# Performance work log

Hardware: AMD Instinct MI355X
Metric: run time of the kernel (lower is better)

## Reference

```python
import jax, jax.numpy as jnp
import numpy as np

N_NODES = 50000
N_EDGES = 800000
IN_DIM = 128
HID_DIM = 128
N_CLASSES = 64


def gcn_conv(x, edge_index, W, b):
    """PyG GCNConv: add self-loops, sym deg^-1/2 norm, xW, scatter-add, +bias."""
    n = x.shape[0]
    loop = jnp.arange(n, dtype=edge_index.dtype)
    src = jnp.concatenate([edge_index[0], loop])  # [E+N]
    dst = jnp.concatenate([edge_index[1], loop])  # [E+N]
    ones = jnp.ones(src.shape[0], dtype=x.dtype)
    deg = jax.ops.segment_sum(ones, dst, num_segments=n)  # in-degree incl self-loop
    dinv = jnp.where(deg > 0, jax.lax.rsqrt(deg), jnp.zeros_like(deg))
    norm = dinv[src] * dinv[dst]  # [E+N]
    h = x @ W  # [N, out]
    msg = h[src] * norm[:, None]  # [E+N, out] gather + scale
    out = jax.ops.segment_sum(msg, dst, num_segments=n)  # scatter-add
    return out + b


def setup_inputs() -> dict:
    key = jax.random.key(0)
    k1, k2, k3, k4, k5 = jax.random.split(key, 5)
    x = jax.random.normal(k1, (N_NODES, IN_DIM), dtype=jnp.float32)
    edge_index = jax.random.randint(k2, (2, N_EDGES), 0, N_NODES, dtype=jnp.int64)
    # Glorot-style init for the two GCNConv linear weights; zero biases (PyG default)
    s1 = 1.0 / np.sqrt(IN_DIM)
    s2 = 1.0 / np.sqrt(HID_DIM)
    W1 = jax.random.uniform(k3, (IN_DIM, HID_DIM), jnp.float32, -s1, s1)
    b1 = jnp.zeros((HID_DIM,), jnp.float32)
    W2 = jax.random.uniform(k4, (HID_DIM, N_CLASSES), jnp.float32, -s2, s2)
    b2 = jnp.zeros((N_CLASSES,), jnp.float32)
    return {"x": x, "edge_index": edge_index, "W1": W1, "b1": b1, "W2": W2, "b2": b2}


def reference(x, edge_index, W1, b1, W2, b2):
    h = gcn_conv(x, edge_index, W1, b1)
    h = jax.nn.relu(h)
    out = gcn_conv(h, edge_index, W2, b2)
    return out
```

## Files before the change

### kernel.cpp

```cpp
#include <hip/hip_runtime.h>
#include <hip/hip_bf16.h>
#include <hip/hip_fp16.h>


#define NODES_PER_BLOCK 4
#define CHUNK 4096
#define BCAP 8192

typedef unsigned int uint;
typedef _Float16 f16x8 __attribute__((ext_vector_type(8)));
typedef float f32x4 __attribute__((ext_vector_type(4)));

__device__ __forceinline__ float2 h2f(uint v) {
  __half2 h;
  __builtin_memcpy(&h, &v, 4);
  return __half22float2(h);
}

__device__ __forceinline__ uint f2h(float a, float b) {
  __half2 h = __halves2half2(__float2half_rn(a), __float2half_rn(b));
  uint r;
  __builtin_memcpy(&r, &h, 4);
  return r;
}

__global__ void detect64_k(const int* ei, int* flag) {
  int lane = threadIdx.x & 63;
  unsigned long long m = __ballot(ei[2 * lane + 1] != 0);
  if (threadIdx.x == 0) *flag = (m == 0ULL) ? 1 : 0;
}

__global__ __launch_bounds__(256) void hist_k(const int* __restrict__ ei,
                                              const int* __restrict__ flag,
                                              int* __restrict__ gh,
                                              int E, int nchunk, int nbuck) {
  __shared__ int h[256];
  int c = blockIdx.x;
  for (int i = threadIdx.x; i < 256; i += 256) h[i] = 0;
  __syncthreads();
  int is64 = *flag;
  int base = c * CHUNK;
  int lim = min(CHUNK, E - base);
  for (int i = threadIdx.x; i < lim; i += 256) {
    int e = base + i;
    int d = is64 ? ei[2 * ((size_t)E + e)] : ei[(size_t)E + e];
    atomicAdd(&h[d >> 8], 1);
  }
  __syncthreads();
  for (int k = threadIdx.x; k < nbuck; k += 256) gh[k * nchunk + c] = h[k];
}

__global__ __launch_bounds__(256) void tot_k(const int* __restrict__ gh,
                                             int* __restrict__ totals, int nchunk) {
  __shared__ int sd[256];
  int k = blockIdx.x;
  int s = 0;
  for (int i = threadIdx.x; i < nchunk; i += 256) s += gh[k * nchunk + i];
  sd[threadIdx.x] = s;
  __syncthreads();
  for (int o = 128; o > 0; o >>= 1) {
    if (threadIdx.x < o) sd[threadIdx.x] += sd[threadIdx.x + o];
    __syncthreads();
  }
  if (threadIdx.x == 0) totals[k] = sd[0];
}

__global__ __launch_bounds__(256) void scanrow_k(int* __restrict__ gh,
                                                 const int* __restrict__ totals,
                                                 int* __restrict__ bucketStart,
                                                 int* __restrict__ offsets,
                                                 int nchunk, int nbuck, int N, int E) {
  __shared__ int st[256];
  int k = blockIdx.x;
  int t = threadIdx.x;
  int v = (t < nbuck && t < k) ? totals[t] : 0;
  st[t] = v;
  __syncthreads();
  for (int o = 128; o > 0; o >>= 1) {
    if (t < o) st[t] += st[t + o];
    __syncthreads();
  }
  int bs = st[0];
  if (t == 0) {
    bucketStart[k] = bs;
    if (k == nbuck - 1) { bucketStart[nbuck] = E; offsets[N] = E; }
  }
  __syncthreads();
  int x = (t < nchunk) ? gh[k * nchunk + t] : 0;
  st[t] = x;
  __syncthreads();
  int incl = x;
  for (int o = 1; o < 256; o <<= 1) {
    int add = (t >= o) ? st[t - o] : 0;
    __syncthreads();
    incl += add;
    st[t] = incl;
    __syncthreads();
  }
  if (t < nchunk) gh[k * nchunk + t] = bs + (incl - x);
}

__global__ __launch_bounds__(256) void part_k(const int* __restrict__ ei,
                                              const int* __restrict__ flag,
                                              const int* __restrict__ gh,
                                              int* __restrict__ tmp,
                                              int E, int nchunk, int nbuck) {
  __shared__ int cur[256];
  int c = blockIdx.x;
  for (int i = threadIdx.x; i < nbuck; i += 256) cur[i] = gh[i * nchunk + c];
  __syncthreads();
  int is64 = *flag;
  int base = c * CHUNK;
  int lim = min(CHUNK, E - base);
  for (int i = threadIdx.x; i < lim; i += 256) {
    int e = base + i;
    int s, d;
    if (is64) {
      s = ei[2 * (size_t)e];
      d = ei[2 * ((size_t)E + e)];
    } else {
      s = ei[e];
      d = ei[(size_t)E + e];
    }
    int p = atomicAdd(&cur[d >> 8], 1);
    tmp[p] = s | ((d & 255) << 16);
  }
}

__global__ __launch_bounds__(256) void bucket_k(const int* __restrict__ tmp,
                                                const int* __restrict__ bucketStart,
                                                int* __restrict__ csr_src,
                                                int* __restrict__ offsets,
                                                float* __restrict__ dinv,
                                                int N) {
  __shared__ int ebuf[BCAP];
  __shared__ int cnt[256];
  __shared__ int st[256];
  __shared__ int lofs[256];
  int k = blockIdx.x;
  int b0 = bucketStart[k], b1 = bucketStart[k + 1];
  int sz = b1 - b0;
  int t = threadIdx.x;
  cnt[t] = 0;
  __syncthreads();
  bool inlds = (sz <= BCAP);
  if (inlds) {
    for (int i = t; i < sz; i += 256) {
      int v = tmp[b0 + i];
      ebuf[i] = v;
      atomicAdd(&cnt[v >> 16], 1);
    }
  } else {
    for (int i = t; i < sz; i += 256) atomicAdd(&cnt[tmp[b0 + i] >> 16], 1);
  }
  __syncthreads();
  int x = cnt[t];
  st[t] = x;
  __syncthreads();
  int incl = x;
  for (int o = 1; o < 256; o <<= 1) {
    int add = (t >= o) ? st[t - o] : 0;
    __syncthreads();
    incl += add;
    st[t] = incl;
    __syncthreads();
  }
  lofs[t] = incl - x;
  int node = k * 256 + t;
  if (node < N) {
    offsets[node] = b0 + lofs[t];
    dinv[node] = rsqrtf((float)(x + 1));
  }
  __syncthreads();
  cnt[t] = lofs[t];
  __syncthreads();
  if (inlds) {
    for (int i = t; i < sz; i += 256) {
      int v = ebuf[i];
      int p = atomicAdd(&cnt[v >> 16], 1);
      csr_src[b0 + p] = v & 0xFFFF;
    }
  } else {
    for (int i = t; i < sz; i += 256) {
      int v = tmp[b0 + i];
      int p = atomicAdd(&cnt[v >> 16], 1);
      csr_src[b0 + p] = v & 0xFFFF;
    }
  }
}

__global__ void prep_k(const float* __restrict__ W, _Float16* __restrict__ P,
                       int NC, int total) {
  int idx = blockIdx.x * blockDim.x + threadIdx.x;
  if (idx >= total) return;
  int NF = NC >> 4;
  int j = idx & 7;
  int l = (idx >> 3) & 63;
  int rest = idx >> 9;
  int c = rest % NF;
  int t = rest / NF;
  int k = t * 32 + ((l >> 4) << 3) + j;
  int col = c * 16 + (l & 15);
  P[idx] = (_Float16)W[(size_t)k * NC + col];
}

template <int NC, bool A16>
__global__ __launch_bounds__(256) void mfma_gemm_k(const void* __restrict__ Xv,
                                                   const _Float16* __restrict__ Wp,
                                                   const float* __restrict__ dinv,
                                                   _Float16* __restrict__ H, int M) {
  constexpr int NF = NC / 16;
  int lane = threadIdx.x & 63;
  int w = threadIdx.x >> 6;
  int row0 = blockIdx.x * 64 + w * 16;
  int arow = row0 + (lane & 15);
  bool av = arow < M;
  const uint4* wp = (const uint4*)Wp;

  f32x4 acc[NF];
#pragma unroll
  for (int c = 0; c < NF; ++c) acc[c] = (f32x4){0.f, 0.f, 0.f, 0.f};

#pragma unroll
  for (int t = 0; t < 4; ++t) {
    f16x8 a;
    if constexpr (A16) {
      const _Float16* xr = (const _Float16*)Xv + (size_t)arow * 128 + ((lane >> 4) << 3);
      uint4 araw = av ? *(const uint4*)(xr + t * 32)
                      : make_uint4(0u, 0u, 0u, 0u);
      __builtin_memcpy(&a, &araw, 16);
    } else {
      const float* xr = (const float*)Xv + (size_t)arow * 128 + ((lane >> 4) << 3);
      float4 lo = av ? *(const float4*)(xr + t * 32)
                     : make_float4(0.f, 0.f, 0.f, 0.f);
      float4 hi = av ? *(const float4*)(xr + t * 32 + 4)
                     : make_float4(0.f, 0.f, 0.f, 0.f);
      a[0] = (_Float16)lo.x; a[1] = (_Float16)lo.y;
      a[2] = (_Float16)lo.z; a[3] = (_Float16)lo.w;
      a[4] = (_Float16)hi.x; a[5] = (_Float16)hi.y;
      a[6] = (_Float16)hi.z; a[7] = (_Float16)hi.w;
    }
#pragma unroll
    for (int c = 0; c < NF; ++c) {
      uint4 braw = wp[(t * NF + c) * 64 + lane];
      f16x8 b;
      __builtin_memcpy(&b, &braw, 16);
      acc[c] = __builtin_amdgcn_mfma_f32_16x16x32_f16(a, b, acc[c], 0, 0, 0);
    }
  }

  int rbase = row0 + ((lane >> 4) << 2);
#pragma unroll
  for (int r = 0; r < 4; ++r) {
    int row = rbase + r;
    if (row < M) {
      float di = dinv[row];
#pragma unroll
      for (int c = 0; c < NF; ++c)
        H[(size_t)row * NC + c * 16 + (lane & 15)] = (_Float16)(di * acc[c][r]);
    }
  }
}

__global__ __launch_bounds__(256) void agg1_k(const uint* __restrict__ hp,
                                              const float* __restrict__ dinv,
                                              const int* __restrict__ offsets,
                                              const int* __restrict__ csr_src,
                                              const float* __restrict__ b,
                                              uint* __restrict__ y, int n) {
  int wave = threadIdx.x >> 6;
  int lane = threadIdx.x & 63;
  int node = blockIdx.x * NODES_PER_BLOCK + wave;
  if (node >= n) return;
  int beg = offsets[node], end = offsets[node + 1];
  int deg = end - beg;
  float2 self = h2f(hp[(size_t)node * 64 + lane]);
  float ax = self.x, ay = self.y;
  int sv = 0;
  if (lane < deg) sv = csr_src[beg + lane];
  int lim = deg < 64 ? deg : 64;
  int e = 0;
  for (; e + 8 <= lim; e += 8) {
    int s0 = __shfl(sv, e + 0), s1 = __shfl(sv, e + 1);
    int s2 = __shfl(sv, e + 2), s3 = __shfl(sv, e + 3);
    int s4 = __shfl(sv, e + 4), s5 = __shfl(sv, e + 5);
    int s6 = __shfl(sv, e + 6), s7 = __shfl(sv, e + 7);
    uint u0 = hp[(size_t)s0 * 64 + lane];
    uint u1 = hp[(size_t)s1 * 64 + lane];
    uint u2 = hp[(size_t)s2 * 64 + lane];
    uint u3 = hp[(size_t)s3 * 64 + lane];
    uint u4 = hp[(size_t)s4 * 64 + lane];
    uint u5 = hp[(size_t)s5 * 64 + lane];
    uint u6 = hp[(size_t)s6 * 64 + lane];
    uint u7 = hp[(size_t)s7 * 64 + lane];
    float2 v0 = h2f(u0), v1 = h2f(u1), v2 = h2f(u2), v3 = h2f(u3);
    float2 v4 = h2f(u4), v5 = h2f(u5), v6 = h2f(u6), v7 = h2f(u7);
    ax += ((v0.x + v1.x) + (v2.x + v3.x)) + ((v4.x + v5.x) + (v6.x + v7.x));
    ay += ((v0.y + v1.y) + (v2.y + v3.y)) + ((v4.y + v5.y) + (v6.y + v7.y));
  }
  for (; e < lim; ++e) {
    int s = __shfl(sv, e);
    float2 v = h2f(hp[(size_t)s * 64 + lane]);
    ax += v.x;
    ay += v.y;
  }
  for (int ee = beg + 64; ee < end; ++ee) {
    float2 v = h2f(hp[(size_t)csr_src[ee] * 64 + lane]);
    ax += v.x;
    ay += v.y;
  }
  float di = dinv[node];
  float2 bb = ((const float2*)b)[lane];
  float ox = fmaxf(fmaf(di, ax, bb.x), 0.0f);
  float oy = fmaxf(fmaf(di, ay, bb.y), 0.0f);
  y[(size_t)node * 64 + lane] = f2h(ox, oy);
}

__global__ __launch_bounds__(256) void agg2_k(const uint* __restrict__ hp,
                                              const float* __restrict__ dinv,
                                              const int* __restrict__ offsets,
                                              const int* __restrict__ csr_src,
                                              const float* __restrict__ b,
                                              float* __restrict__ out, int n) {
  int wv = threadIdx.x >> 6;
  int lane = threadIdx.x & 63;
  int half = lane >> 5;
  int fl = lane & 31;
  int node = blockIdx.x * 8 + wv * 2 + half;
  if (node >= n) return;
  int beg = offsets[node], end = offsets[node + 1];
  int deg = end - beg;
  float2 self = h2f(hp[(size_t)node * 32 + fl]);
  float ax = self.x, ay = self.y;
  int sv = 0;
  if (fl < deg) sv = csr_src[beg + fl];
  int lim = deg < 32 ? deg : 32;
  int e = 0;
  for (; e + 8 <= lim; e += 8) {
    int s0 = __shfl(sv, e + 0, 32), s1 = __shfl(sv, e + 1, 32);
    int s2 = __shfl(sv, e + 2, 32), s3 = __shfl(sv, e + 3, 32);
    int s4 = __shfl(sv, e + 4, 32), s5 = __shfl(sv, e + 5, 32);
    int s6 = __shfl(sv, e + 6, 32), s7 = __shfl(sv, e + 7, 32);
    uint u0 = hp[(size_t)s0 * 32 + fl];
    uint u1 = hp[(size_t)s1 * 32 + fl];
    uint u2 = hp[(size_t)s2 * 32 + fl];
    uint u3 = hp[(size_t)s3 * 32 + fl];
    uint u4 = hp[(size_t)s4 * 32 + fl];
    uint u5 = hp[(size_t)s5 * 32 + fl];
    uint u6 = hp[(size_t)s6 * 32 + fl];
    uint u7 = hp[(size_t)s7 * 32 + fl];
    float2 v0 = h2f(u0), v1 = h2f(u1), v2 = h2f(u2), v3 = h2f(u3);
    float2 v4 = h2f(u4), v5 = h2f(u5), v6 = h2f(u6), v7 = h2f(u7);
    ax += ((v0.x + v1.x) + (v2.x + v3.x)) + ((v4.x + v5.x) + (v6.x + v7.x));
    ay += ((v0.y + v1.y) + (v2.y + v3.y)) + ((v4.y + v5.y) + (v6.y + v7.y));
  }
  for (; e < lim; ++e) {
    int s = __shfl(sv, e, 32);
    float2 v = h2f(hp[(size_t)s * 32 + fl]);
    ax += v.x;
    ay += v.y;
  }
  for (int ee = beg + 32; ee < end; ++ee) {
    float2 v = h2f(hp[(size_t)csr_src[ee] * 32 + fl]);
    ax += v.x;
    ay += v.y;
  }
  float di = dinv[node];
  float2 bb = ((const float2*)b)[fl];
  float2 o;
  o.x = fmaf(di, ax, bb.x);
  o.y = fmaf(di, ay, bb.y);
  ((float2*)out)[(size_t)node * 32 + fl] = o;
}

extern "C" void kernel_launch(void* const* d_in, const int* in_sizes, int n_in,
                              void* d_out, int out_size, void* d_ws, size_t ws_size,
                              hipStream_t stream) {
  const float* x  = (const float*)d_in[0];
  const int*   ei = (const int*)d_in[1];
  const float* W1 = (const float*)d_in[2];
  const float* b1 = (const float*)d_in[3];
  const float* W2 = (const float*)d_in[4];
  const float* b2 = (const float*)d_in[5];
  float* out = (float*)d_out;

  const int N = in_sizes[0] / 128;
  const int E = in_sizes[1] / 2;
  const int NBUCK = (N + 255) >> 8;
  const int NCHUNK = (E + CHUNK - 1) / CHUNK;

  char* w = (char*)d_ws;
  size_t off = 0;
  auto alloc = [&](size_t bytes) -> void* {
    void* p = w + off;
    off = (off + bytes + 511) & ~(size_t)511;
    return p;
  };
  int*       gh      = (int*)alloc((size_t)NBUCK * NCHUNK * 4);
  int*       totals  = (int*)alloc((size_t)NBUCK * 4);
  int*       bstart  = (int*)alloc((size_t)(NBUCK + 1) * 4);
  int*       flag    = (int*)alloc(64);
  int*       tmp     = (int*)alloc((size_t)E * 4);
  int*       offsets = (int*)alloc((size_t)(N + 1) * 4);
  float*     dinv    = (float*)alloc((size_t)N * 4);
  int*       csr_src = (int*)alloc((size_t)E * 4);
  _Float16*  pW1     = (_Float16*)alloc(16384 * 2);
  _Float16*  pW2     = (_Float16*)alloc(8192 * 2);
  _Float16*  h1      = (_Float16*)alloc((size_t)N * 128 * 2);
  _Float16*  y       = (_Float16*)alloc((size_t)N * 128 * 2);
  _Float16*  h2      = (_Float16*)alloc((size_t)N * 64 * 2);

  const int GB  = (N + 63) / 64;
  const int AB  = (N + NODES_PER_BLOCK - 1) / NODES_PER_BLOCK;
  const int AB2 = (N + 7) / 8;

  detect64_k<<<1, 64, 0, stream>>>(ei, flag);
  hist_k<<<NCHUNK, 256, 0, stream>>>(ei, flag, gh, E, NCHUNK, NBUCK);
  tot_k<<<NBUCK, 256, 0, stream>>>(gh, totals, NCHUNK);
  scanrow_k<<<NBUCK, 256, 0, stream>>>(gh, totals, bstart, offsets, NCHUNK, NBUCK, N, E);
  part_k<<<NCHUNK, 256, 0, stream>>>(ei, flag, gh, tmp, E, NCHUNK, NBUCK);
  bucket_k<<<NBUCK, 256, 0, stream>>>(tmp, bstart, csr_src, offsets, dinv, N);

  prep_k<<<64, 256, 0, stream>>>(W1, pW1, 128, 16384);
  prep_k<<<32, 256, 0, stream>>>(W2, pW2, 64, 8192);

  mfma_gemm_k<128, false><<<GB, 256, 0, stream>>>(x, pW1, dinv, h1, N);
  agg1_k<<<AB, 256, 0, stream>>>((const uint*)h1, dinv, offsets, csr_src, b1,
                                 (uint*)y, N);
  mfma_gemm_k<64, true><<<GB, 256, 0, stream>>>(y, pW2, dinv, h2, N);
  agg2_k<<<AB2, 256, 0, stream>>>((const uint*)h2, dinv, offsets, csr_src, b2, out, N);
}
```

Measured before the change: 118.0 us.

## Column-chunk feature layout for aggregation, smaller buckets, fuse detect and prep kernels

Stores the GEMM outputs in 32-column chunks (chunk-major), so each gather row is 64 bytes and the chunks can be aggregated by separate blocks. A single templated aggregation kernel replaces the two old ones: four lane groups each handle a different edge and are combined with shuffles. CSR bucket size drops from 256 to 128 nodes, the int64 detection is folded into hist and part, and the two weight-prep kernels are merged. This cuts launch count and spreads the gather over more blocks, at the cost of more grid blocks and extra shuffle reductions.

```diff
diff --git a/kernel.cpp b/kernel.cpp
--- a/kernel.cpp
+++ b/kernel.cpp
@@ -3,9 +3,10 @@
 #include <hip/hip_fp16.h>
 
 
-#define NODES_PER_BLOCK 4
 #define CHUNK 4096
-#define BCAP 8192
+#define BSHIFT 7
+#define BSIZE 128
+#define BCAP 4096
 
 typedef unsigned int uint;
 typedef _Float16 f16x8 __attribute__((ext_vector_type(8)));
@@ -24,27 +25,29 @@
   return r;
 }
 
-__global__ void detect64_k(const int* ei, int* flag) {
-  int lane = threadIdx.x & 63;
-  unsigned long long m = __ballot(ei[2 * lane + 1] != 0);
-  if (threadIdx.x == 0) *flag = (m == 0ULL) ? 1 : 0;
+__device__ __forceinline__ int block_is64(const int* ei, int* s_is64) {
+  if (threadIdx.x < 64) {
+    unsigned long long m = __ballot(ei[2 * threadIdx.x + 1] != 0);
+    if (threadIdx.x == 0) *s_is64 = (m == 0ULL) ? 1 : 0;
+  }
+  __syncthreads();
+  return *s_is64;
 }
 
 __global__ __launch_bounds__(256) void hist_k(const int* __restrict__ ei,
-                                              const int* __restrict__ flag,
                                               int* __restrict__ gh,
                                               int E, int nchunk, int nbuck) {
-  __shared__ int h[256];
+  __shared__ int h[512];
+  __shared__ int s_is64;
   int c = blockIdx.x;
-  for (int i = threadIdx.x; i < 256; i += 256) h[i] = 0;
-  __syncthreads();
-  int is64 = *flag;
+  for (int i = threadIdx.x; i < 512; i += 256) h[i] = 0;
+  int is64 = block_is64(ei, &s_is64);
   int base = c * CHUNK;
   int lim = min(CHUNK, E - base);
   for (int i = threadIdx.x; i < lim; i += 256) {
     int e = base + i;
     int d = is64 ? ei[2 * ((size_t)E + e)] : ei[(size_t)E + e];
-    atomicAdd(&h[d >> 8], 1);
+    atomicAdd(&h[d >> BSHIFT], 1);
   }
   __syncthreads();
   for (int k = threadIdx.x; k < nbuck; k += 256) gh[k * nchunk + c] = h[k];
@@ -73,8 +76,9 @@
   __shared__ int st[256];
   int k = blockIdx.x;
   int t = threadIdx.x;
-  int v = (t < nbuck && t < k) ? totals[t] : 0;
-  st[t] = v;
+  int partial = 0;
+  for (int i = t; i < k; i += 256) partial += totals[i];
+  st[t] = partial;
   __syncthreads();
   for (int o = 128; o > 0; o >>= 1) {
     if (t < o) st[t] += st[t + o];
@@ -101,15 +105,14 @@
 }
 
 __global__ __launch_bounds__(256) void part_k(const int* __restrict__ ei,
-                                              const int* __restrict__ flag,
                                               const int* __restrict__ gh,
                                               int* __restrict__ tmp,
                                               int E, int nchunk, int nbuck) {
-  __shared__ int cur[256];
+  __shared__ int cur[512];
+  __shared__ int s_is64;
   int c = blockIdx.x;
   for (int i = threadIdx.x; i < nbuck; i += 256) cur[i] = gh[i * nchunk + c];
-  __syncthreads();
-  int is64 = *flag;
+  int is64 = block_is64(ei, &s_is64);
   int base = c * CHUNK;
   int lim = min(CHUNK, E - base);
   for (int i = threadIdx.x; i < lim; i += 256) {
@@ -122,8 +125,8 @@
       s = ei[e];
       d = ei[(size_t)E + e];
     }
-    int p = atomicAdd(&cur[d >> 8], 1);
-    tmp[p] = s | ((d & 255) << 16);
+    int p = atomicAdd(&cur[d >> BSHIFT], 1);
+    tmp[p] = s | ((d & (BSIZE - 1)) << 16);
   }
 }
 
@@ -134,14 +137,14 @@
                                                 float* __restrict__ dinv,
                                                 int N) {
   __shared__ int ebuf[BCAP];
-  __shared__ int cnt[256];
+  __shared__ int cnt[BSIZE];
   __shared__ int st[256];
-  __shared__ int lofs[256];
+  __shared__ int lofs[BSIZE];
   int k = blockIdx.x;
   int b0 = bucketStart[k], b1 = bucketStart[k + 1];
   int sz = b1 - b0;
   int t = threadIdx.x;
-  cnt[t] = 0;
+  if (t < BSIZE) cnt[t] = 0;
   __syncthreads();
   bool inlds = (sz <= BCAP);
   if (inlds) {
@@ -154,7 +157,7 @@
     for (int i = t; i < sz; i += 256) atomicAdd(&cnt[tmp[b0 + i] >> 16], 1);
   }
   __syncthreads();
-  int x = cnt[t];
+  int x = (t < BSIZE) ? cnt[t] : 0;
   st[t] = x;
   __syncthreads();
   int incl = x;
@@ -165,14 +168,16 @@
     st[t] = incl;
     __syncthreads();
   }
-  lofs[t] = incl - x;
-  int node = k * 256 + t;
-  if (node < N) {
-    offsets[node] = b0 + lofs[t];
-    dinv[node] = rsqrtf((float)(x + 1));
-  }
-  __syncthreads();
-  cnt[t] = lofs[t];
+  int node = (k << BSHIFT) + t;
+  if (t < BSIZE) {
+    lofs[t] = incl - x;
+    if (node < N) {
+      offsets[node] = b0 + lofs[t];
+      dinv[node] = rsqrtf((float)(x + 1));
+    }
+  }
+  __syncthreads();
+  if (t < BSIZE) cnt[t] = lofs[t];
   __syncthreads();
   if (inlds) {
     for (int i = t; i < sz; i += 256) {
@@ -189,19 +194,25 @@
   }
 }
 
-__global__ void prep_k(const float* __restrict__ W, _Float16* __restrict__ P,
-                       int NC, int total) {
+__global__ void prep2_k(const float* __restrict__ W1,
+                        const float* __restrict__ W2,
+                        _Float16* __restrict__ P) {
   int idx = blockIdx.x * blockDim.x + threadIdx.x;
-  if (idx >= total) return;
+  if (idx >= 24576) return;
+  const float* W;
+  _Float16* dst;
+  int NC, li;
+  if (idx < 16384) { W = W1; dst = P;        NC = 128; li = idx; }
+  else             { W = W2; dst = P + 16384; NC = 64;  li = idx - 16384; }
   int NF = NC >> 4;
-  int j = idx & 7;
-  int l = (idx >> 3) & 63;
-  int rest = idx >> 9;
+  int j = li & 7;
+  int l = (li >> 3) & 63;
+  int rest = li >> 9;
   int c = rest % NF;
   int t = rest / NF;
   int k = t * 32 + ((l >> 4) << 3) + j;
   int col = c * 16 + (l & 15);
-  P[idx] = (_Float16)W[(size_t)k * NC + col];
+  dst[li] = (_Float16)W[(size_t)k * NC + col];
 }
 
 template <int NC, bool A16>
@@ -225,16 +236,15 @@
   for (int t = 0; t < 4; ++t) {
     f16x8 a;
     if constexpr (A16) {
-      const _Float16* xr = (const _Float16*)Xv + (size_t)arow * 128 + ((lane >> 4) << 3);
-      uint4 araw = av ? *(const uint4*)(xr + t * 32)
-                      : make_uint4(0u, 0u, 0u, 0u);
+      const _Float16* yr =
+          (const _Float16*)Xv + ((size_t)t * M + arow) * 32 + ((lane >> 4) << 3);
+      uint4 araw = av ? *(const uint4*)yr : make_uint4(0u, 0u, 0u, 0u);
       __builtin_memcpy(&a, &araw, 16);
     } else {
-      const float* xr = (const float*)Xv + (size_t)arow * 128 + ((lane >> 4) << 3);
-      float4 lo = av ? *(const float4*)(xr + t * 32)
-                     : make_float4(0.f, 0.f, 0.f, 0.f);
-      float4 hi = av ? *(const float4*)(xr + t * 32 + 4)
-                     : make_float4(0.f, 0.f, 0.f, 0.f);
+      const float* xr =
+          (const float*)Xv + (size_t)arow * 128 + ((lane >> 4) << 3) + t * 32;
+      float4 lo = av ? *(const float4*)xr : make_float4(0.f, 0.f, 0.f, 0.f);
+      float4 hi = av ? *(const float4*)(xr + 4) : make_float4(0.f, 0.f, 0.f, 0.f);
       a[0] = (_Float16)lo.x; a[1] = (_Float16)lo.y;
       a[2] = (_Float16)lo.z; a[3] = (_Float16)lo.w;
       a[4] = (_Float16)hi.x; a[5] = (_Float16)hi.y;
@@ -256,121 +266,82 @@
     if (row < M) {
       float di = dinv[row];
 #pragma unroll
-      for (int c = 0; c < NF; ++c)
-        H[(size_t)row * NC + c * 16 + (lane & 15)] = (_Float16)(di * acc[c][r]);
-    }
-  }
-}
-
-__global__ __launch_bounds__(256) void agg1_k(const uint* __restrict__ hp,
-                                              const float* __restrict__ dinv,
-                                              const int* __restrict__ offsets,
-                                              const int* __restrict__ csr_src,
-                                              const float* __restrict__ b,
-                                              uint* __restrict__ y, int n) {
+      for (int c = 0; c < NF; ++c) {
+        size_t off = ((size_t)(c >> 1) * M + row) * 32 + (c & 1) * 16 + (lane & 15);
+        H[off] = (_Float16)(di * acc[c][r]);
+      }
+    }
+  }
+}
+
+template <bool RELU, bool OUT16>
+__global__ __launch_bounds__(256) void agg_k(const uint* __restrict__ hp,
+                                             const float* __restrict__ dinv,
+                                             const int* __restrict__ offsets,
+                                             const int* __restrict__ csr_src,
+                                             const float* __restrict__ b,
+                                             void* __restrict__ outv,
+                                             int n, int nblk, int ncfull) {
   int wave = threadIdx.x >> 6;
   int lane = threadIdx.x & 63;
-  int node = blockIdx.x * NODES_PER_BLOCK + wave;
+  int c = blockIdx.x / nblk;
+  int nb = blockIdx.x % nblk;
+  int node = nb * 4 + wave;
   if (node >= n) return;
+  int g = lane >> 4;
+  int j = lane & 15;
   int beg = offsets[node], end = offsets[node + 1];
   int deg = end - beg;
-  float2 self = h2f(hp[(size_t)node * 64 + lane]);
-  float ax = self.x, ay = self.y;
+  const uint* hc = hp + (size_t)c * n * 16;
+  float ax = 0.f, ay = 0.f;
+  if (g == 0) {
+    float2 s = h2f(hc[(size_t)node * 16 + j]);
+    ax = s.x; ay = s.y;
+  }
   int sv = 0;
   if (lane < deg) sv = csr_src[beg + lane];
   int lim = deg < 64 ? deg : 64;
-  int e = 0;
-  for (; e + 8 <= lim; e += 8) {
-    int s0 = __shfl(sv, e + 0), s1 = __shfl(sv, e + 1);
-    int s2 = __shfl(sv, e + 2), s3 = __shfl(sv, e + 3);
-    int s4 = __shfl(sv, e + 4), s5 = __shfl(sv, e + 5);
-    int s6 = __shfl(sv, e + 6), s7 = __shfl(sv, e + 7);
-    uint u0 = hp[(size_t)s0 * 64 + lane];
-    uint u1 = hp[(size_t)s1 * 64 + lane];
-    uint u2 = hp[(size_t)s2 * 64 + lane];
-    uint u3 = hp[(size_t)s3 * 64 + lane];
-    uint u4 = hp[(size_t)s4 * 64 + lane];
-    uint u5 = hp[(size_t)s5 * 64 + lane];
-    uint u6 = hp[(size_t)s6 * 64 + lane];
-    uint u7 = hp[(size_t)s7 * 64 + lane];
-    float2 v0 = h2f(u0), v1 = h2f(u1), v2 = h2f(u2), v3 = h2f(u3);
-    float2 v4 = h2f(u4), v5 = h2f(u5), v6 = h2f(u6), v7 = h2f(u7);
-    ax += ((v0.x + v1.x) + (v2.x + v3.x)) + ((v4.x + v5.x) + (v6.x + v7.x));
-    ay += ((v0.y + v1.y) + (v2.y + v3.y)) + ((v4.y + v5.y) + (v6.y + v7.y));
-  }
-  for (; e < lim; ++e) {
-    int s = __shfl(sv, e);
-    float2 v = h2f(hp[(size_t)s * 64 + lane]);
-    ax += v.x;
-    ay += v.y;
-  }
-  for (int ee = beg + 64; ee < end; ++ee) {
-    float2 v = h2f(hp[(size_t)csr_src[ee] * 64 + lane]);
-    ax += v.x;
-    ay += v.y;
-  }
-  float di = dinv[node];
-  float2 bb = ((const float2*)b)[lane];
-  float ox = fmaxf(fmaf(di, ax, bb.x), 0.0f);
-  float oy = fmaxf(fmaf(di, ay, bb.y), 0.0f);
-  y[(size_t)node * 64 + lane] = f2h(ox, oy);
-}
-
-__global__ __launch_bounds__(256) void agg2_k(const uint* __restrict__ hp,
-                                              const float* __restrict__ dinv,
-                                              const int* __restrict__ offsets,
-                                              const int* __restrict__ csr_src,
-                                              const float* __restrict__ b,
-                                              float* __restrict__ out, int n) {
-  int wv = threadIdx.x >> 6;
-  int lane = threadIdx.x & 63;
-  int half = lane >> 5;
-  int fl = lane & 31;
-  int node = blockIdx.x * 8 + wv * 2 + half;
-  if (node >= n) return;
-  int beg = offsets[node], end = offsets[node + 1];
-  int deg = end - beg;
-  float2 self = h2f(hp[(size_t)node * 32 + fl]);
-  float ax = self.x, ay = self.y;
-  int sv = 0;
-  if (fl < deg) sv = csr_src[beg + fl];
-  int lim = deg < 32 ? deg : 32;
-  int e = 0;
-  for (; e + 8 <= lim; e += 8) {
-    int s0 = __shfl(sv, e + 0, 32), s1 = __shfl(sv, e + 1, 32);
-    int s2 = __shfl(sv, e + 2, 32), s3 = __shfl(sv, e + 3, 32);
-    int s4 = __shfl(sv, e + 4, 32), s5 = __shfl(sv, e + 5, 32);
-    int s6 = __shfl(sv, e + 6, 32), s7 = __shfl(sv, e + 7, 32);
-    uint u0 = hp[(size_t)s0 * 32 + fl];
-    uint u1 = hp[(size_t)s1 * 32 + fl];
-    uint u2 = hp[(size_t)s2 * 32 + fl];
-    uint u3 = hp[(size_t)s3 * 32 + fl];
-    uint u4 = hp[(size_t)s4 * 32 + fl];
-    uint u5 = hp[(size_t)s5 * 32 + fl];
-    uint u6 = hp[(size_t)s6 * 32 + fl];
-    uint u7 = hp[(size_t)s7 * 32 + fl];
-    float2 v0 = h2f(u0), v1 = h2f(u1), v2 = h2f(u2), v3 = h2f(u3);
-    float2 v4 = h2f(u4), v5 = h2f(u5), v6 = h2f(u6), v7 = h2f(u7);
-    ax += ((v0.x + v1.x) + (v2.x + v3.x)) + ((v4.x + v5.x) + (v6.x + v7.x));
-    ay += ((v0.y + v1.y) + (v2.y + v3.y)) + ((v4.y + v5.y) + (v6.y + v7.y));
-  }
-  for (; e < lim; ++e) {
-    int s = __shfl(sv, e, 32);
-    float2 v = h2f(hp[(size_t)s * 32 + fl]);
-    ax += v.x;
-    ay += v.y;
-  }
-  for (int ee = beg + 32; ee < end; ++ee) {
-    float2 v = h2f(hp[(size_t)csr_src[ee] * 32 + fl]);
-    ax += v.x;
-    ay += v.y;
-  }
-  float di = dinv[node];
-  float2 bb = ((const float2*)b)[fl];
-  float2 o;
-  o.x = fmaf(di, ax, bb.x);
-  o.y = fmaf(di, ay, bb.y);
-  ((float2*)out)[(size_t)node * 32 + fl] = o;
+  int e0 = 0;
+  for (; e0 + 8 <= lim; e0 += 8) {
+    int sA = __shfl(sv, e0 + g);
+    int sB = __shfl(sv, e0 + 4 + g);
+    uint uA = hc[(size_t)sA * 16 + j];
+    uint uB = hc[(size_t)sB * 16 + j];
+    float2 vA = h2f(uA), vB = h2f(uB);
+    ax += vA.x + vB.x;
+    ay += vA.y + vB.y;
+  }
+  for (; e0 < lim; e0 += 4) {
+    int idx = e0 + g;
+    bool val = idx < lim;
+    int s = __shfl(sv, val ? idx : 0);
+    if (val) {
+      float2 v = h2f(hc[(size_t)s * 16 + j]);
+      ax += v.x; ay += v.y;
+    }
+  }
+  for (int ee = beg + 64; ee < end; ee += 4) {
+    int idx = ee + g;
+    if (idx < end) {
+      float2 v = h2f(hc[(size_t)csr_src[idx] * 16 + j]);
+      ax += v.x; ay += v.y;
+    }
+  }
+  ax += __shfl_xor(ax, 16); ay += __shfl_xor(ay, 16);
+  ax += __shfl_xor(ax, 32); ay += __shfl_xor(ay, 32);
+  if (g == 0) {
+    float di = dinv[node];
+    float2 bb = ((const float2*)b)[c * 16 + j];
+    float ox = fmaf(di, ax, bb.x);
+    float oy = fmaf(di, ay, bb.y);
+    if (RELU) { ox = fmaxf(ox, 0.f); oy = fmaxf(oy, 0.f); }
+    if (OUT16) {
+      ((uint*)outv)[((size_t)c * n + node) * 16 + j] = f2h(ox, oy);
+    } else {
+      ((float2*)outv)[(size_t)node * (ncfull >> 1) + c * 16 + j] =
+          make_float2(ox, oy);
+    }
+  }
 }
 
 extern "C" void kernel_launch(void* const* d_in, const int* in_sizes, int n_in,
@@ -386,7 +357,7 @@
 
   const int N = in_sizes[0] / 128;
   const int E = in_sizes[1] / 2;
-  const int NBUCK = (N + 255) >> 8;
+  const int NBUCK = (N + BSIZE - 1) >> BSHIFT;
   const int NCHUNK = (E + CHUNK - 1) / CHUNK;
 
   char* w = (char*)d_ws;
@@ -399,34 +370,30 @@
   int*       gh      = (int*)alloc((size_t)NBUCK * NCHUNK * 4);
   int*       totals  = (int*)alloc((size_t)NBUCK * 4);
   int*       bstart  = (int*)alloc((size_t)(NBUCK + 1) * 4);
-  int*       flag    = (int*)alloc(64);
   int*       tmp     = (int*)alloc((size_t)E * 4);
   int*       offsets = (int*)alloc((size_t)(N + 1) * 4);
   float*     dinv    = (float*)alloc((size_t)N * 4);
   int*       csr_src = (int*)alloc((size_t)E * 4);
-  _Float16*  pW1     = (_Float16*)alloc(16384 * 2);
-  _Float16*  pW2     = (_Float16*)alloc(8192 * 2);
+  _Float16*  pW      = (_Float16*)alloc(24576 * 2);
   _Float16*  h1      = (_Float16*)alloc((size_t)N * 128 * 2);
   _Float16*  y       = (_Float16*)alloc((size_t)N * 128 * 2);
   _Float16*  h2      = (_Float16*)alloc((size_t)N * 64 * 2);
 
-  const int GB  = (N + 63) / 64;
-  const int AB  = (N + NODES_PER_BLOCK - 1) / NODES_PER_BLOCK;
-  const int AB2 = (N + 7) / 8;
-
-  detect64_k<<<1, 64, 0, stream>>>(ei, flag);
-  hist_k<<<NCHUNK, 256, 0, stream>>>(ei, flag, gh, E, NCHUNK, NBUCK);
+  const int GB   = (N + 63) / 64;
+  const int NBLK = (N + 3) / 4;
+
+  hist_k<<<NCHUNK, 256, 0, stream>>>(ei, gh, E, NCHUNK, NBUCK);
   tot_k<<<NBUCK, 256, 0, stream>>>(gh, totals, NCHUNK);
   scanrow_k<<<NBUCK, 256, 0, stream>>>(gh, totals, bstart, offsets, NCHUNK, NBUCK, N, E);
-  part_k<<<NCHUNK, 256, 0, stream>>>(ei, flag, gh, tmp, E, NCHUNK, NBUCK);
+  part_k<<<NCHUNK, 256, 0, stream>>>(ei, gh, tmp, E, NCHUNK, NBUCK);
   bucket_k<<<NBUCK, 256, 0, stream>>>(tmp, bstart, csr_src, offsets, dinv, N);
 
-  prep_k<<<64, 256, 0, stream>>>(W1, pW1, 128, 16384);
-  prep_k<<<32, 256, 0, stream>>>(W2, pW2, 64, 8192);
-
-  mfma_gemm_k<128, false><<<GB, 256, 0, stream>>>(x, pW1, dinv, h1, N);
-  agg1_k<<<AB, 256, 0, stream>>>((const uint*)h1, dinv, offsets, csr_src, b1,
-                                 (uint*)y, N);
-  mfma_gemm_k<64, true><<<GB, 256, 0, stream>>>(y, pW2, dinv, h2, N);
-  agg2_k<<<AB2, 256, 0, stream>>>((const uint*)h2, dinv, offsets, csr_src, b2, out, N);
-}
+  prep2_k<<<96, 256, 0, stream>>>(W1, W2, pW);
+
+  mfma_gemm_k<128, false><<<GB, 256, 0, stream>>>(x, pW, dinv, h1, N);
+  agg_k<true, true><<<4 * NBLK, 256, 0, stream>>>((const uint*)h1, dinv, offsets,
+                                                  csr_src, b1, y, N, NBLK, 128);
+  mfma_gemm_k<64, true><<<GB, 256, 0, stream>>>(y, pW + 16384, dinv, h2, N);
+  agg_k<false, false><<<2 * NBLK, 256, 0, stream>>>((const uint*)h2, dinv, offsets,
+                                                    csr_src, b2, out, N, NBLK, 64);
+}
```

Result: slower. 163.7 us (+38.8%).
